# Performance work log

Measured on AMD Instinct MI355X. Metric: run time of the kernel, lower is better.

## Reference

```python
import jax, jax.numpy as jnp
import numpy as np

N_NODES = 100000
N_EDGES = 1600000
IN_F = 128
HID = 128
OUT_F = 8
N_GRAPHS = 512


def setup_inputs() -> dict:
    key = jax.random.key(0)
    ks = jax.random.split(key, 12)
    x = jax.random.normal(ks[0], (N_NODES, IN_F), dtype=jnp.float32)
    edge_index = jax.random.randint(ks[1], (2, N_EDGES), 0, N_NODES, dtype=jnp.int64)
    edge_attr = jax.random.uniform(ks[2], (N_EDGES,), dtype=jnp.float32)
    batch = jnp.sort(jax.random.randint(ks[3], (N_NODES,), 0, N_GRAPHS, dtype=jnp.int64))
    # GCNConv weights (glorot-ish scaling) and biases
    def lin(k, fi, fo):
        return jax.random.normal(k, (fi, fo), dtype=jnp.float32) / np.sqrt(fi)
    W1 = lin(ks[4], IN_F, HID); b1 = jnp.zeros((HID,), jnp.float32)
    W2 = lin(ks[5], HID, HID); b2 = jnp.zeros((HID,), jnp.float32)
    W3 = lin(ks[6], HID, HID); b3 = jnp.zeros((HID,), jnp.float32)
    Wlin = lin(ks[7], HID, OUT_F)
    blin = jnp.zeros((OUT_F,), jnp.float32)
    return {"x": x, "edge_index": edge_index, "edge_attr": edge_attr, "batch": batch,
            "W1": W1, "b1": b1, "W2": W2, "b2": b2, "W3": W3, "b3": b3,
            "Wlin": Wlin, "blin": blin}


def _gcn_layer(x, src, dst, norm_e, norm_self, W, b):
    # h = X W;  out_i = sum_{j->i} norm_e * h_j  +  norm_self_i * h_i  + b
    h = x @ W
    msgs = h[src] * norm_e[:, None]                      # [E, F] gather + scale
    agg = jax.ops.segment_sum(msgs, dst, num_segments=x.shape[0])
    agg = agg + h * norm_self[:, None]                   # self-loop contribution
    return agg + b


def reference(x, edge_index, edge_attr, batch, W1, b1, W2, b2, W3, b3, Wlin, blin):
    src, dst = edge_index[0], edge_index[1]
    n = x.shape[0]
    # GCN symmetric normalization with added self-loops (weight 1)
    deg = jax.ops.segment_sum(jnp.ones_like(src, dtype=x.dtype), dst, num_segments=n) + 1.0
    dinv = jax.lax.rsqrt(deg)
    norm_e = dinv[src] * dinv[dst]                        # per-edge coeff
    norm_self = dinv * dinv                               # self-loop coeff

    h = _gcn_layer(x, src, dst, norm_e, norm_self, W1, b1)
    h = jax.nn.relu(h)
    h = _gcn_layer(h, src, dst, norm_e, norm_self, W2, b2)
    h = jax.nn.relu(h)
    h = _gcn_layer(h, src, dst, norm_e, norm_self, W3, b3)  # no relu on last conv

    # global_mean_pool over graph ids
    sums = jax.ops.segment_sum(h, batch, num_segments=N_GRAPHS)
    counts = jax.ops.segment_sum(jnp.ones((n,), h.dtype), batch, num_segments=N_GRAPHS)
    pooled = sums / jnp.maximum(counts, 1.0)[:, None]

    # dropout is identity at inference
    logits = pooled @ Wlin + blin
    return logits
```

## Files before the change

### kernel.cpp

```cpp
#include <hip/hip_runtime.h>
#include <hip/hip_fp16.h>


#define THREADS 256


__global__ __launch_bounds__(THREADS) void k_deg(const int* __restrict__ dst,
                                                 int* __restrict__ degi, int E) {
  int e = blockIdx.x * THREADS + threadIdx.x;
  if (e < E) atomicAdd(&degi[dst[e]], 1);
}

__global__ __launch_bounds__(THREADS) void k_cntbs(const int* __restrict__ batch,
                                                   float* __restrict__ cnts,
                                                   int N, int G) {
  int g = blockIdx.x * THREADS + threadIdx.x;
  if (g >= G) return;
  int lo = 0, hi = N;
  while (lo < hi) {
    int mid = (lo + hi) >> 1;
    if (batch[mid] < g) lo = mid + 1; else hi = mid;
  }
  int lb0 = lo;
  lo = 0; hi = N;
  while (lo < hi) {
    int mid = (lo + hi) >> 1;
    if (batch[mid] < g + 1) lo = mid + 1; else hi = mid;
  }
  cnts[g] = (float)(lo - lb0);
}

__global__ __launch_bounds__(THREADS) void k_rsq(const int* __restrict__ degi,
                                                 float* __restrict__ dinv, int N) {
  int i = blockIdx.x * THREADS + threadIdx.x;
  if (i < N) dinv[i] = rsqrtf((float)degi[i] + 1.0f);
}


__global__ __launch_bounds__(THREADS) void k_scan1(const int* __restrict__ degi,
                                                   int* __restrict__ rowptr,
                                                   int* __restrict__ bsum, int N) {
  __shared__ int s[THREADS];
  int i = blockIdx.x * THREADS + threadIdx.x;
  int v = (i < N) ? degi[i] : 0;
  s[threadIdx.x] = v;
  __syncthreads();
#pragma unroll
  for (int off = 1; off < THREADS; off <<= 1) {
    int t = (threadIdx.x >= off) ? s[threadIdx.x - off] : 0;
    __syncthreads();
    s[threadIdx.x] += t;
    __syncthreads();
  }
  if (i < N) rowptr[i] = s[threadIdx.x] - v;
  if (threadIdx.x == THREADS - 1) bsum[blockIdx.x] = s[THREADS - 1];
}

__global__ __launch_bounds__(512) void k_scan2(int* __restrict__ bsum, int nb) {
  __shared__ int s[512];
  int v = (threadIdx.x < nb) ? bsum[threadIdx.x] : 0;
  s[threadIdx.x] = v;
  __syncthreads();
#pragma unroll
  for (int off = 1; off < 512; off <<= 1) {
    int t = (threadIdx.x >= off) ? s[threadIdx.x - off] : 0;
    __syncthreads();
    s[threadIdx.x] += t;
    __syncthreads();
  }
  if (threadIdx.x < nb) bsum[threadIdx.x] = s[threadIdx.x] - v;
}

__global__ __launch_bounds__(THREADS) void k_scan3(int* __restrict__ rowptr,
                                                   const int* __restrict__ bsum,
                                                   int N, int E) {
  int i = blockIdx.x * THREADS + threadIdx.x;
  if (i < N) rowptr[i] += bsum[blockIdx.x];
  if (i == 0) rowptr[N] = E;
}


__global__ __launch_bounds__(THREADS) void k_csr(const int* __restrict__ src,
                                                 const int* __restrict__ dst,
                                                 const int* __restrict__ rowptr,
                                                 int* __restrict__ cursor,
                                                 const float* __restrict__ dinv,
                                                 int2* __restrict__ rec, int E) {
  int e = blockIdx.x * THREADS + threadIdx.x;
  if (e >= E) return;
  int s = src[e];
  int d = dst[e];
  int pos = atomicAdd(&cursor[d], 1);
  int idx = rowptr[d] + pos;
  float w = dinv[s] * dinv[d];
  union {
    int2 v;
    unsigned long long u;
  } cv;
  cv.v = make_int2(s, __float_as_int(w));
  __builtin_nontemporal_store(cv.u, (unsigned long long*)&rec[idx]);
}


__global__ __launch_bounds__(THREADS) void k_wcomb(const float* __restrict__ W3,
                                                   const float* __restrict__ Wl,
                                                   const float* __restrict__ b3,
                                                   const float* __restrict__ bl,
                                                   float* __restrict__ Wc,
                                                   float* __restrict__ bc) {
  int idx = blockIdx.x * THREADS + threadIdx.x;
  if (idx < 1024) {
    int k = idx >> 3, o = idx & 7;
    float a = 0.f;
#pragma unroll 8
    for (int j = 0; j < 128; ++j) a = fmaf(W3[k * 128 + j], Wl[j * 8 + o], a);
    Wc[idx] = a;
  }
  if (idx < 8) {
    float a = bl[idx];
    for (int j = 0; j < 128; ++j) a = fmaf(b3[j], Wl[j * 8 + idx], a);
    bc[idx] = a;
  }
}


__device__ inline float4 ldrow4(const float* __restrict__ p) {
  return *(const float4*)p;
}

__device__ inline float4 ldrow4(const __half* __restrict__ p) {
  float2 raw = *(const float2*)p;
  const __half2* h = (const __half2*)&raw;
  float2 a = __half22float2(h[0]);
  float2 b = __half22float2(h[1]);
  return make_float4(a.x, a.y, b.x, b.y);
}

struct f8 { float v[8]; };

__device__ inline f8 ld_h8(const __half* __restrict__ p) {
  float4 raw = *(const float4*)p;
  const __half2* h = (const __half2*)&raw;
  float2 a = __half22float2(h[0]);
  float2 b = __half22float2(h[1]);
  float2 c = __half22float2(h[2]);
  float2 d = __half22float2(h[3]);
  f8 o;
  o.v[0] = a.x; o.v[1] = a.y; o.v[2] = b.x; o.v[3] = b.y;
  o.v[4] = c.x; o.v[5] = c.y; o.v[6] = d.x; o.v[7] = d.y;
  return o;
}

__device__ inline void st_nt_h4(__half* __restrict__ p, float x, float y,
                                float z, float w) {
  union {
    __half2 h2[2];
    unsigned long long u;
  } cv;
  cv.h2[0] = __floats2half2_rn(x, y);
  cv.h2[1] = __floats2half2_rn(z, w);
  __builtin_nontemporal_store(cv.u, (unsigned long long*)p);
}


template <typename T>
__global__ __launch_bounds__(THREADS) void k_gemm128(const T* __restrict__ X,
                                                     const float* __restrict__ W,
                                                     __half* __restrict__ H16, int M) {
  __shared__ float4 sW[128 * 32];
  const int t = threadIdx.x;
#pragma unroll
  for (int i = 0; i < 16; ++i) sW[t + i * 256] = ((const float4*)W)[t + i * 256];
  __syncthreads();

  const int tx = t & 31;
  const int ty = t >> 5;
  const int r0 = blockIdx.x * 64 + ty * 8;

  const T* xp[8];
#pragma unroll
  for (int i = 0; i < 8; ++i) {
    int r = r0 + i;
    if (r >= M) r = M - 1;
    xp[i] = X + (size_t)r * 128;
  }

  float4 acc[8];
#pragma unroll
  for (int i = 0; i < 8; ++i) acc[i] = make_float4(0.f, 0.f, 0.f, 0.f);

#pragma unroll 2
  for (int k = 0; k < 128; k += 4) {
    float4 xv[8];
#pragma unroll
    for (int i = 0; i < 8; ++i) xv[i] = ldrow4(xp[i] + k);
#pragma unroll
    for (int kk = 0; kk < 4; ++kk) {
      float4 w = sW[(k + kk) * 32 + tx];
#pragma unroll
      for (int i = 0; i < 8; ++i) {
        float xs = (kk == 0) ? xv[i].x : (kk == 1) ? xv[i].y : (kk == 2) ? xv[i].z : xv[i].w;
        acc[i].x = fmaf(xs, w.x, acc[i].x);
        acc[i].y = fmaf(xs, w.y, acc[i].y);
        acc[i].z = fmaf(xs, w.z, acc[i].z);
        acc[i].w = fmaf(xs, w.w, acc[i].w);
      }
    }
  }

#pragma unroll
  for (int i = 0; i < 8; ++i) {
    int r = r0 + i;
    if (r < M)
      st_nt_h4(H16 + (size_t)r * 128 + tx * 4, acc[i].x, acc[i].y, acc[i].z, acc[i].w);
  }
}


__global__ __launch_bounds__(THREADS) void k_gemm8(const __half* __restrict__ B16,
                                                   const float* __restrict__ Wc,
                                                   float* __restrict__ P3, int M) {
  __shared__ float sWc[1024];
#pragma unroll
  for (int i = 0; i < 4; ++i) sWc[threadIdx.x + i * 256] = Wc[threadIdx.x + i * 256];
  __syncthreads();

  int i = blockIdx.x * THREADS + threadIdx.x;
  if (i >= M) return;

  float acc[8];
#pragma unroll
  for (int o = 0; o < 8; ++o) acc[o] = 0.f;

  const __half* row = B16 + (size_t)i * 128;
#pragma unroll 4
  for (int k = 0; k < 128; k += 8) {
    f8 x = ld_h8(row + k);
#pragma unroll
    for (int u = 0; u < 8; ++u) {
      const float* wr = &sWc[(k + u) * 8];
#pragma unroll
      for (int o = 0; o < 8; ++o) acc[o] = fmaf(x.v[u], wr[o], acc[o]);
    }
  }
  float4* out = (float4*)(P3 + (size_t)i * 8);
  out[0] = make_float4(acc[0], acc[1], acc[2], acc[3]);
  out[1] = make_float4(acc[4], acc[5], acc[6], acc[7]);
}


__global__ __launch_bounds__(THREADS) void k_gather(const __half* __restrict__ H16,
                                                    const int* __restrict__ rowptr,
                                                    const int2* __restrict__ rec,
                                                    const float* __restrict__ dinv,
                                                    const float* __restrict__ bias,
                                                    __half* __restrict__ B16, int N) {
  int gid = blockIdx.x * THREADS + threadIdx.x;
  int i = gid >> 5;
  int lane = gid & 31;
  if (i >= N) return;
  int beg = rowptr[i];
  int end = rowptr[i + 1];

  float4 acc = make_float4(0.f, 0.f, 0.f, 0.f);
  int k = beg;
  for (; k + 3 < end; k += 4) {
    int2 r0 = rec[k],     r1 = rec[k + 1];
    int2 r2 = rec[k + 2], r3 = rec[k + 3];
    float4 h0 = ldrow4(H16 + (size_t)r0.x * 128 + lane * 4);
    float4 h1 = ldrow4(H16 + (size_t)r1.x * 128 + lane * 4);
    float4 h2 = ldrow4(H16 + (size_t)r2.x * 128 + lane * 4);
    float4 h3 = ldrow4(H16 + (size_t)r3.x * 128 + lane * 4);
    float w0 = __int_as_float(r0.y), w1 = __int_as_float(r1.y);
    float w2 = __int_as_float(r2.y), w3 = __int_as_float(r3.y);
    acc.x = fmaf(w0, h0.x, acc.x); acc.y = fmaf(w0, h0.y, acc.y);
    acc.z = fmaf(w0, h0.z, acc.z); acc.w = fmaf(w0, h0.w, acc.w);
    acc.x = fmaf(w1, h1.x, acc.x); acc.y = fmaf(w1, h1.y, acc.y);
    acc.z = fmaf(w1, h1.z, acc.z); acc.w = fmaf(w1, h1.w, acc.w);
    acc.x = fmaf(w2, h2.x, acc.x); acc.y = fmaf(w2, h2.y, acc.y);
    acc.z = fmaf(w2, h2.z, acc.z); acc.w = fmaf(w2, h2.w, acc.w);
    acc.x = fmaf(w3, h3.x, acc.x); acc.y = fmaf(w3, h3.y, acc.y);
    acc.z = fmaf(w3, h3.z, acc.z); acc.w = fmaf(w3, h3.w, acc.w);
  }
  for (; k < end; ++k) {
    int2 r0 = rec[k];
    float w0 = __int_as_float(r0.y);
    float4 h0 = ldrow4(H16 + (size_t)r0.x * 128 + lane * 4);
    acc.x = fmaf(w0, h0.x, acc.x); acc.y = fmaf(w0, h0.y, acc.y);
    acc.z = fmaf(w0, h0.z, acc.z); acc.w = fmaf(w0, h0.w, acc.w);
  }

  float di = dinv[i];
  float ns = di * di;
  float4 hs = ldrow4(H16 + (size_t)i * 128 + lane * 4);
  float4 bb = *(const float4*)(bias + lane * 4);
  float4 v;
  v.x = fmaxf(fmaf(hs.x, ns, acc.x) + bb.x, 0.f);
  v.y = fmaxf(fmaf(hs.y, ns, acc.y) + bb.y, 0.f);
  v.z = fmaxf(fmaf(hs.z, ns, acc.z) + bb.z, 0.f);
  v.w = fmaxf(fmaf(hs.w, ns, acc.w) + bb.w, 0.f);
  st_nt_h4(B16 + (size_t)i * 128 + lane * 4, v.x, v.y, v.z, v.w);
}


__global__ __launch_bounds__(THREADS) void k_gather_pool(const float* __restrict__ P3,
                                                         const int* __restrict__ rowptr,
                                                         const int2* __restrict__ rec,
                                                         const float* __restrict__ dinv,
                                                         const int* __restrict__ batch,
                                                         float* __restrict__ pooled,
                                                         int N) {
  int gid = blockIdx.x * THREADS + threadIdx.x;
  int i = gid >> 3;
  int lane = gid & 7;
  if (i >= N) return;
  int beg = rowptr[i];
  int end = rowptr[i + 1];

  float acc = 0.f;
  int k = beg;
  for (; k + 1 < end; k += 2) {
    int2 ra = rec[k], rb = rec[k + 1];
    float pa = P3[(size_t)ra.x * 8 + lane];
    float pb = P3[(size_t)rb.x * 8 + lane];
    acc = fmaf(__int_as_float(ra.y), pa, acc);
    acc = fmaf(__int_as_float(rb.y), pb, acc);
  }
  if (k < end) {
    int2 ra = rec[k];
    acc = fmaf(__int_as_float(ra.y), P3[(size_t)ra.x * 8 + lane], acc);
  }

  float dd = dinv[i];
  acc = fmaf(dd * dd, P3[(size_t)i * 8 + lane], acc);

  atomicAdd(&pooled[(size_t)batch[i] * 8 + lane], acc);
}


__global__ __launch_bounds__(THREADS) void k_head(const float* __restrict__ pooled,
                                                  const float* __restrict__ cnts,
                                                  const float* __restrict__ bc,
                                                  float* __restrict__ out, int G) {
  int gid = blockIdx.x * THREADS + threadIdx.x;
  int g = gid >> 3;
  int o = gid & 7;
  if (g >= G) return;
  out[g * 8 + o] = pooled[g * 8 + o] / fmaxf(cnts[g], 1.0f) + bc[o];
}


extern "C" void kernel_launch(void* const* d_in, const int* in_sizes, int n_in,
                              void* d_out, int out_size, void* d_ws, size_t ws_size,
                              hipStream_t stream) {
  const float* x     = (const float*)d_in[0];
  const int*   ei    = (const int*)d_in[1];
  const int*   batch = (const int*)d_in[3];
  const float* W1 = (const float*)d_in[4];
  const float* b1 = (const float*)d_in[5];
  const float* W2 = (const float*)d_in[6];
  const float* b2 = (const float*)d_in[7];
  const float* W3 = (const float*)d_in[8];
  const float* b3 = (const float*)d_in[9];
  const float* Wl = (const float*)d_in[10];
  const float* bl = (const float*)d_in[11];
  float* out = (float*)d_out;

  const int N = in_sizes[0] / 128;
  const int E = in_sizes[1] / 2;
  const int G = out_size / 8;
  const int* srcp = ei;
  const int* dstp = ei + E;

  char* ws = (char*)d_ws;
  __half* H16 = (__half*)ws;
  __half* B16 = H16 + (size_t)N * 128;
  float*  P3  = (float*)(B16 + (size_t)N * 128);
  int*   degi   = (int*)(P3 + (size_t)N * 8);
  int*   cursor = degi + N;
  float* pooled = (float*)(cursor + N);
  float* cnts    = pooled + (size_t)G * 8;
  float* dinv    = cnts + G;
  float* Wc      = dinv + N;
  float* bc      = Wc + 1024;
  int*   rowptr  = (int*)(bc + 8);
  int*   bsum    = rowptr + N + 1;
  int2*  rec     = (int2*)(bsum + 2048);

  const size_t zero_bytes = ((size_t)2 * N + (size_t)G * 8) * sizeof(float);
  (void)hipMemsetAsync(degi, 0, zero_bytes, stream);

  const int nbE = (E + THREADS - 1) / THREADS;
  const int nbN = (N + THREADS - 1) / THREADS;

  k_deg<<<nbE, THREADS, 0, stream>>>(dstp, degi, E);
  k_cntbs<<<(G + THREADS - 1) / THREADS, THREADS, 0, stream>>>(batch, cnts, N, G);
  k_rsq<<<nbN, THREADS, 0, stream>>>(degi, dinv, N);
  k_scan1<<<nbN, THREADS, 0, stream>>>(degi, rowptr, bsum, N);
  k_scan2<<<1, 512, 0, stream>>>(bsum, nbN);
  k_scan3<<<nbN, THREADS, 0, stream>>>(rowptr, bsum, N, E);
  k_csr<<<nbE, THREADS, 0, stream>>>(srcp, dstp, rowptr, cursor, dinv, rec, E);
  k_wcomb<<<4, THREADS, 0, stream>>>(W3, Wl, b3, bl, Wc, bc);

  const int gemm_blocks = (N + 63) / 64;
  const int gat_blocks = (int)(((long long)N * 32 + THREADS - 1) / THREADS);
  const int gp_blocks = (int)(((long long)N * 8 + THREADS - 1) / THREADS);

  k_gemm128<float><<<gemm_blocks, THREADS, 0, stream>>>(x, W1, H16, N);
  k_gather<<<gat_blocks, THREADS, 0, stream>>>(H16, rowptr, rec, dinv, b1, B16, N);
  k_gemm128<__half><<<gemm_blocks, THREADS, 0, stream>>>(B16, W2, H16, N);
  k_gather<<<gat_blocks, THREADS, 0, stream>>>(H16, rowptr, rec, dinv, b2, B16, N);
  k_gemm8<<<nbN, THREADS, 0, stream>>>(B16, Wc, P3, N);
  k_gather_pool<<<gp_blocks, THREADS, 0, stream>>>(P3, rowptr, rec, dinv, batch, pooled, N);

  k_head<<<(G * 8 + THREADS - 1) / THREADS, THREADS, 0, stream>>>(pooled, cnts, bc, out, G);
}
```

Measured before the change: 510.2 us.

## Build CSR via two-pass bucketed placement to localize scattered writes

Replaces the single-pass CSR build, which scattered edge records to random destination rows, with two passes. The first pass counts edges per coarse bucket of 128 destination nodes and places (src,dst) pairs into a bucket-ordered staging buffer. The second pass then scatters within buckets, so atomics and writes land in nearby memory. This adds an extra pass over E edges, a staging buffer, more atomics on a few bucket counters (contention), and a single-block scan that assumes at most 1024 buckets.

```diff
diff --git a/kernel.cpp b/kernel.cpp
--- a/kernel.cpp
+++ b/kernel.cpp
@@ -3,12 +3,18 @@
 
 
 #define THREADS 256
+#define BSHIFT 7
 
 
 __global__ __launch_bounds__(THREADS) void k_deg(const int* __restrict__ dst,
-                                                 int* __restrict__ degi, int E) {
+                                                 int* __restrict__ degi,
+                                                 int* __restrict__ bcnt, int E) {
   int e = blockIdx.x * THREADS + threadIdx.x;
-  if (e < E) atomicAdd(&degi[dst[e]], 1);
+  if (e < E) {
+    int d = dst[e];
+    atomicAdd(&degi[d], 1);
+    atomicAdd(&bcnt[d >> BSHIFT], 1);
+  }
 }
 
 __global__ __launch_bounds__(THREADS) void k_cntbs(const int* __restrict__ batch,
@@ -79,26 +85,50 @@
   if (i == 0) rowptr[N] = E;
 }
 
-
-__global__ __launch_bounds__(THREADS) void k_csr(const int* __restrict__ src,
-                                                 const int* __restrict__ dst,
-                                                 const int* __restrict__ rowptr,
-                                                 int* __restrict__ cursor,
-                                                 const float* __restrict__ dinv,
-                                                 int2* __restrict__ rec, int E) {
+__global__ __launch_bounds__(1024) void k_bscan(const int* __restrict__ bcnt,
+                                                int* __restrict__ bbase, int NB) {
+  __shared__ int s[1024];
+  int v = ((int)threadIdx.x < NB) ? bcnt[threadIdx.x] : 0;
+  s[threadIdx.x] = v;
+  __syncthreads();
+#pragma unroll
+  for (int off = 1; off < 1024; off <<= 1) {
+    int t = (threadIdx.x >= (unsigned)off) ? s[threadIdx.x - off] : 0;
+    __syncthreads();
+    s[threadIdx.x] += t;
+    __syncthreads();
+  }
+  if ((int)threadIdx.x < NB) bbase[threadIdx.x] = s[threadIdx.x] - v;
+}
+
+
+__global__ __launch_bounds__(THREADS) void k_bplace(const int* __restrict__ src,
+                                                    const int* __restrict__ dst,
+                                                    const int* __restrict__ bbase,
+                                                    int* __restrict__ bcur,
+                                                    int2* __restrict__ stage, int E) {
   int e = blockIdx.x * THREADS + threadIdx.x;
   if (e >= E) return;
   int s = src[e];
   int d = dst[e];
-  int pos = atomicAdd(&cursor[d], 1);
-  int idx = rowptr[d] + pos;
-  float w = dinv[s] * dinv[d];
-  union {
-    int2 v;
-    unsigned long long u;
-  } cv;
-  cv.v = make_int2(s, __float_as_int(w));
-  __builtin_nontemporal_store(cv.u, (unsigned long long*)&rec[idx]);
+  int b = d >> BSHIFT;
+  int pos = atomicAdd(&bcur[b], 1);
+  stage[bbase[b] + pos] = make_int2(s, d);
+}
+
+
+__global__ __launch_bounds__(THREADS) void k_csr2(const int2* __restrict__ stage,
+                                                  const int* __restrict__ rowptr,
+                                                  int* __restrict__ cursor,
+                                                  const float* __restrict__ dinv,
+                                                  int2* __restrict__ rec, int E) {
+  int i = blockIdx.x * THREADS + threadIdx.x;
+  if (i >= E) return;
+  int2 sd = stage[i];
+  int pos = atomicAdd(&cursor[sd.y], 1);
+  int idx = rowptr[sd.y] + pos;
+  float w = dinv[sd.x] * dinv[sd.y];
+  rec[idx] = make_int2(sd.x, __float_as_int(w));
 }
 
 
@@ -369,6 +399,7 @@
   const int N = in_sizes[0] / 128;
   const int E = in_sizes[1] / 2;
   const int G = out_size / 8;
+  const int NB = (N >> BSHIFT) + 1;
   const int* srcp = ei;
   const int* dstp = ei + E;
 
@@ -378,28 +409,34 @@
   float*  P3  = (float*)(B16 + (size_t)N * 128);
   int*   degi   = (int*)(P3 + (size_t)N * 8);
   int*   cursor = degi + N;
-  float* pooled = (float*)(cursor + N);
+  int*   bcnt   = cursor + N;
+  int*   bcur   = bcnt + 1024;
+  float* pooled = (float*)(bcur + 1024);
   float* cnts    = pooled + (size_t)G * 8;
   float* dinv    = cnts + G;
   float* Wc      = dinv + N;
   float* bc      = Wc + 1024;
   int*   rowptr  = (int*)(bc + 8);
   int*   bsum    = rowptr + N + 1;
-  int2*  rec     = (int2*)(bsum + 2048);
-
-  const size_t zero_bytes = ((size_t)2 * N + (size_t)G * 8) * sizeof(float);
+  int*   bbase   = bsum + 2048;
+  int2*  rec     = (int2*)(bbase + 1024);
+  int2*  stage   = rec + E;
+
+  const size_t zero_bytes = ((size_t)2 * N + 2048 + (size_t)G * 8) * sizeof(int);
   (void)hipMemsetAsync(degi, 0, zero_bytes, stream);
 
   const int nbE = (E + THREADS - 1) / THREADS;
   const int nbN = (N + THREADS - 1) / THREADS;
 
-  k_deg<<<nbE, THREADS, 0, stream>>>(dstp, degi, E);
+  k_deg<<<nbE, THREADS, 0, stream>>>(dstp, degi, bcnt, E);
   k_cntbs<<<(G + THREADS - 1) / THREADS, THREADS, 0, stream>>>(batch, cnts, N, G);
   k_rsq<<<nbN, THREADS, 0, stream>>>(degi, dinv, N);
   k_scan1<<<nbN, THREADS, 0, stream>>>(degi, rowptr, bsum, N);
   k_scan2<<<1, 512, 0, stream>>>(bsum, nbN);
   k_scan3<<<nbN, THREADS, 0, stream>>>(rowptr, bsum, N, E);
-  k_csr<<<nbE, THREADS, 0, stream>>>(srcp, dstp, rowptr, cursor, dinv, rec, E);
+  k_bscan<<<1, 1024, 0, stream>>>(bcnt, bbase, NB);
+  k_bplace<<<nbE, THREADS, 0, stream>>>(srcp, dstp, bbase, bcur, stage, E);
+  k_csr2<<<nbE, THREADS, 0, stream>>>(stage, rowptr, cursor, dinv, rec, E);
   k_wcomb<<<4, THREADS, 0, stream>>>(W3, Wl, b3, bl, Wc, bc);
 
   const int gemm_blocks = (N + 63) / 64;
```

Result: slower. 1.213 ms (+137.8%).
